# Kernel tuning notes

Measured on AMD Instinct MI355X. Metric: run time of the kernel, lower is better.

The kernel has to match this reference:

```python
import jax, jax.numpy as jnp
import numpy as np

WINDOW = 7
TOKEN_SELF_ATTN_VALUE = -5e4  # from lucidrains local-attention
LN_EPS = 1e-5


def _layer_norm(x, g, b):
    mu = jnp.mean(x, axis=-1, keepdims=True)
    var = jnp.mean(jnp.square(x - mu), axis=-1, keepdims=True)
    return (x - mu) * jax.lax.rsqrt(var + LN_EPS) * g + b


def _local_attention(q, k, v, window):
    # q,k,v: (b, n, d); shared_qk=True, causal=True, look_backward=1, look_forward=0
    b, n, d = q.shape
    nw = n // window
    scale = d ** -0.5
    # shared_qk: l2-normalize keys (torch F.normalize eps=1e-12)
    k = k / jnp.maximum(jnp.linalg.norm(k, axis=-1, keepdims=True), 1e-12)
    bq = q.reshape(b, nw, window, d) * scale
    bk = k.reshape(b, nw, window, d)
    bv = v.reshape(b, nw, window, d)
    # look_around: previous window + current window -> (b, nw, 2w, d)
    prev_k = jnp.pad(bk, ((0, 0), (1, 0), (0, 0), (0, 0)))[:, :nw]
    prev_v = jnp.pad(bv, ((0, 0), (1, 0), (0, 0), (0, 0)))[:, :nw]
    bk2 = jnp.concatenate([prev_k, bk], axis=2)
    bv2 = jnp.concatenate([prev_v, bv], axis=2)
    # absolute positions; padded positions marked -1
    t = jnp.arange(n).reshape(nw, window)             # (nw, w)
    prev_t = jnp.pad(t, ((1, 0), (0, 0)), constant_values=-1)[:nw]
    tk = jnp.concatenate([prev_t, t], axis=1)          # (nw, 2w)
    sim = jnp.einsum('bnie,bnje->bnij', bq, bk2)       # (b, nw, w, 2w)
    self_mask = t[:, :, None] == tk[:, None, :]
    sim = jnp.where(self_mask, TOKEN_SELF_ATTN_VALUE, sim)
    invalid = (t[:, :, None] < tk[:, None, :]) | (tk[:, None, :] == -1)
    sim = jnp.where(invalid, -jnp.finfo(sim.dtype).max, sim)
    attn = jax.nn.softmax(sim, axis=-1)
    out = jnp.einsum('bnij,bnjd->bnid', attn, bv2)
    return out.reshape(b, n, d)


def setup_inputs() -> dict:
    key = jax.random.key(0)
    ks = jax.random.split(key, 10)
    B, H, W, C = 8, 112, 112, 256
    s = 1.0 / np.sqrt(C)
    return {
        'x': jax.random.normal(ks[0], (B, H, W, C), dtype=jnp.float32),
        'ln_g': jnp.ones((C,), jnp.float32),
        'ln_b': jnp.zeros((C,), jnp.float32),
        'wq_w': jax.random.uniform(ks[1], (C, C), jnp.float32, -s, s),
        'wq_b': jax.random.uniform(ks[2], (C,), jnp.float32, -s, s),
        'wk_w': jax.random.uniform(ks[3], (C, C), jnp.float32, -s, s),
        'wk_b': jax.random.uniform(ks[4], (C,), jnp.float32, -s, s),
        'wv_w': jax.random.uniform(ks[5], (C, C), jnp.float32, -s, s),
        'wv_b': jax.random.uniform(ks[6], (C,), jnp.float32, -s, s),
        'mlp_w': jax.random.uniform(ks[7], (C, C), jnp.float32, -s, s),
        'mlp_b': jax.random.uniform(ks[8], (C,), jnp.float32, -s, s),
    }


def reference(x, ln_g, ln_b, wq_w, wq_b, wk_w, wk_b, wv_w, wv_b, mlp_w, mlp_b):
    B, H, W, C = x.shape
    shift = WINDOW // 2  # int(7/2) = 3
    xs = jnp.roll(x, (shift, shift), axis=(1, 2))
    xs = _layer_norm(xs, ln_g, ln_b)
    flat = xs.reshape(B, H * W, C)
    q = flat @ wq_w.T + wq_b
    k = flat @ wk_w.T + wk_b
    v = flat @ wv_w.T + wv_b
    attn_out = _local_attention(q, k, v, WINDOW).reshape(B, H, W, C)
    x_unshifted = jnp.roll(attn_out, (-shift, -shift), axis=(1, 2))
    residual = x_unshifted + x
    xn = _layer_norm(residual, ln_g, ln_b)  # same LN params (module reused)
    flat2 = xn.reshape(B, H * W, C)
    mlp = jax.nn.gelu(flat2 @ mlp_w.T + mlp_b, approximate=False).reshape(B, H, W, C)
    return mlp + residual
```

## Files before the change

kernel.cpp:

```cpp
#include <hip/hip_runtime.h>

#define NTOK 100352
#define NPB  12544
#define CH   256

typedef unsigned short u16;
typedef float f32x4 __attribute__((ext_vector_type(4)));
typedef short bfrag __attribute__((ext_vector_type(8)));

static __device__ __forceinline__ u16 f2bf(float f) {
    union { float f; unsigned u; } v; v.f = f;
    unsigned r = v.u + 0x7FFFu + ((v.u >> 16) & 1u);
    return (u16)(r >> 16);
}
static __device__ __forceinline__ float bf2f(u16 h) {
    union { unsigned u; float f; } v; v.u = ((unsigned)h) << 16;
    return v.f;
}
static __device__ __forceinline__ unsigned pk2(float a, float b) {
    return (unsigned)f2bf(a) | ((unsigned)f2bf(b) << 16);
}
static __device__ __forceinline__ void gl16(const u16* g, u16* l) {
    __builtin_amdgcn_global_load_lds(
        (const __attribute__((address_space(1))) void*)g,
        (__attribute__((address_space(3))) void*)l, 16, 0, 0);
}
static __device__ __forceinline__ float gelu_fast(float v) {
    float z = v * 0.70710678118654752f;
    float a = fabsf(z);
    float t = 1.0f / fmaf(0.3275911f, a, 1.0f);
    float p = t * fmaf(t, fmaf(t, fmaf(t, fmaf(t, 1.061405429f, -1.453152027f),
                                        1.421413741f), -0.284496736f), 0.254829592f);
    float e = __expf(-a * a);
    float erfa = fmaf(-p, e, 1.0f);
    float erfz = (z < 0.f) ? -erfa : erfa;
    return 0.5f * v * (1.0f + erfz);
}

__global__ __launch_bounds__(256)
void swa_prep(const float* __restrict__ wq, const float* __restrict__ wk,
              const float* __restrict__ wv, const float* __restrict__ wm,
              u16* __restrict__ wcat, u16* __restrict__ wmb)
{
    int i0 = blockIdx.x * 256 + threadIdx.x;
    int stride = gridDim.x * 256;
    for (int i = i0; i < 768 * 256; i += stride) {
        int r = i >> 8, c = i & 255;
        float v;
        if (r < 256)      v = wq[r * 256 + c] * 0.0625f;
        else if (r < 512) v = wk[(r - 256) * 256 + c];
        else              v = wv[(r - 512) * 256 + c];
        wcat[i] = f2bf(v);
    }
    for (int i = i0; i < 256 * 256; i += stride) wmb[i] = f2bf(wm[i]);
}

__global__ __launch_bounds__(256)
void swa_ln(const float* __restrict__ x,
            const float* __restrict__ ln_g, const float* __restrict__ ln_b,
            u16* __restrict__ xn)
{
    const int lane = threadIdx.x & 63;
    const int wid  = threadIdx.x >> 6;
    f32x4 lg = *reinterpret_cast<const f32x4*>(ln_g + lane * 4);
    f32x4 lb = *reinterpret_cast<const f32x4*>(ln_b + lane * 4);

    const int wtok0 = (blockIdx.x * 4 + wid) * 16;
    for (int i = 0; i < 16; ++i) {
        int tok = wtok0 + i;
        int b_  = tok / NPB;
        int rem = tok - b_ * NPB;
        int h = rem / 112, w = rem - h * 112;
        int h0 = h - 3 + ((h < 3) ? 112 : 0);
        int w0 = w - 3 + ((w < 3) ? 112 : 0);
        f32x4 v = *reinterpret_cast<const f32x4*>(x + (size_t)(b_ * NPB + h0 * 112 + w0) * CH + lane * 4);
        float s  = v[0] + v[1] + v[2] + v[3];
        float sq = v[0]*v[0] + v[1]*v[1] + v[2]*v[2] + v[3]*v[3];
        #pragma unroll
        for (int m = 1; m < 64; m <<= 1) { s += __shfl_xor(s, m); sq += __shfl_xor(sq, m); }
        float mu  = s * (1.0f / 256.0f);
        float var = sq * (1.0f / 256.0f) - mu * mu;
        float inv = 1.0f / sqrtf(var + 1e-5f);
        uint2 p;
        p.x = pk2((v[0] - mu) * inv * lg[0] + lb[0], (v[1] - mu) * inv * lg[1] + lb[1]);
        p.y = pk2((v[2] - mu) * inv * lg[2] + lb[2], (v[3] - mu) * inv * lg[3] + lb[3]);
        *reinterpret_cast<uint2*>(xn + (size_t)tok * CH + lane * 4) = p;
    }
}

__global__ __launch_bounds__(512)
void swa_kv(const u16* __restrict__ xn, const u16* __restrict__ wcat,
            const float* __restrict__ bk, const float* __restrict__ bv,
            u16* __restrict__ kbuf, u16* __restrict__ vbuf)
{
    __shared__ u16 wt[128 * 256];

    const int tid  = threadIdx.x;
    const int lane = tid & 63;
    const int wid  = tid >> 6;
    const int r16  = lane & 15, g4 = lane >> 4;
    const int swz   = (blockIdx.x & 7) * 196 + (blockIdx.x >> 3);
    const int type  = swz / 392;
    const int strip = swz % 392;
    const int sec   = 1 + (type >> 1);
    const int half  = type & 1;
    const int tok0w = strip * 256 + wid * 32;
    const int wrow0 = sec * 256 + half * 128;

    #pragma unroll
    for (int rr2 = 0; rr2 < 8; ++rr2) {
        int o   = (tid + rr2 * 512) * 16;
        int row = o >> 9;
        int cp  = (o >> 4) & 31;
        int c   = (cp & 24) | ((cp & 7) ^ (row & 7));
        gl16(wcat + (size_t)(wrow0 + row) * CH + c * 8, wt + o / 2);
    }

    bfrag bx[2][8];
    #pragma unroll
    for (int fj = 0; fj < 2; ++fj) {
        const u16* xp = xn + (size_t)(tok0w + fj * 16 + r16) * CH + g4 * 8;
        #pragma unroll
        for (int kb = 0; kb < 8; ++kb)
            bx[fj][kb] = *reinterpret_cast<const bfrag*>(xp + kb * 32);
    }

    u16*         outp = (sec == 1) ? kbuf : vbuf;
    const float* bsp  = (sec == 1) ? bk : bv;

    __syncthreads();

    #pragma unroll
    for (int p = 0; p < 4; ++p) {
        f32x4 acc[2][2];
        #pragma unroll
        for (int ct = 0; ct < 2; ++ct) { acc[ct][0] = (f32x4)0.f; acc[ct][1] = (f32x4)0.f; }
        #pragma unroll
        for (int kk = 0; kk < 8; ++kk) {
            bfrag af[2];
            #pragma unroll
            for (int ct = 0; ct < 2; ++ct) {
                int row = p * 32 + ct * 16 + r16;
                int cc  = kk * 4 + g4;
                int cp  = (cc & 24) | ((cc & 7) ^ (row & 7));
                af[ct]  = *reinterpret_cast<const bfrag*>((const char*)wt + row * 512 + cp * 16);
            }
            #pragma unroll
            for (int ct = 0; ct < 2; ++ct) {
                acc[ct][0] = __builtin_amdgcn_mfma_f32_16x16x32_bf16(af[ct], bx[0][kk], acc[ct][0], 0, 0, 0);
                acc[ct][1] = __builtin_amdgcn_mfma_f32_16x16x32_bf16(af[ct], bx[1][kk], acc[ct][1], 0, 0, 0);
            }
        }
        #pragma unroll
        for (int ct = 0; ct < 2; ++ct) {
            int ch = half * 128 + p * 32 + ct * 16 + g4 * 4;
            f32x4 bb = *reinterpret_cast<const f32x4*>(bsp + ch);
            #pragma unroll
            for (int fj = 0; fj < 2; ++fj) {
                int tok = tok0w + fj * 16 + r16;
                uint2 pkk;
                pkk.x = pk2(acc[ct][fj][0] + bb[0], acc[ct][fj][1] + bb[1]);
                pkk.y = pk2(acc[ct][fj][2] + bb[2], acc[ct][fj][3] + bb[3]);
                *reinterpret_cast<uint2*>(outp + (size_t)tok * CH + ch) = pkk;
            }
        }
    }
}

__global__ __launch_bounds__(512)
void swa_q(u16* xnq, const u16* __restrict__ wcat, const float* __restrict__ bq)
{
    __shared__ u16 wt[256 * 256];

    const int tid  = threadIdx.x;
    const int lane = tid & 63;
    const int wid  = tid >> 6;
    const int r16  = lane & 15, g4 = lane >> 4;
    const int strip = (blockIdx.x & 7) * 49 + (blockIdx.x >> 3);
    const int tok0w = strip * 256 + wid * 32;

    #pragma unroll
    for (int rr2 = 0; rr2 < 16; ++rr2) {
        int o   = (tid + rr2 * 512) * 16;
        int row = o >> 9;
        int cp  = (o >> 4) & 31;
        int c   = (cp & 24) | ((cp & 7) ^ (row & 7));
        gl16(wcat + (size_t)row * CH + c * 8, wt + o / 2);
    }

    bfrag bx[2][8];
    #pragma unroll
    for (int fj = 0; fj < 2; ++fj) {
        const u16* xp = xnq + (size_t)(tok0w + fj * 16 + r16) * CH + g4 * 8;
        #pragma unroll
        for (int kb = 0; kb < 8; ++kb)
            bx[fj][kb] = *reinterpret_cast<const bfrag*>(xp + kb * 32);
    }

    __syncthreads();

    #pragma unroll
    for (int p = 0; p < 8; ++p) {
        f32x4 acc[2][2];
        #pragma unroll
        for (int ct = 0; ct < 2; ++ct) { acc[ct][0] = (f32x4)0.f; acc[ct][1] = (f32x4)0.f; }
        #pragma unroll
        for (int kk = 0; kk < 8; ++kk) {
            bfrag af[2];
            #pragma unroll
            for (int ct = 0; ct < 2; ++ct) {
                int row = p * 32 + ct * 16 + r16;
                int cc  = kk * 4 + g4;
                int cp  = (cc & 24) | ((cc & 7) ^ (row & 7));
                af[ct]  = *reinterpret_cast<const bfrag*>((const char*)wt + row * 512 + cp * 16);
            }
            #pragma unroll
            for (int ct = 0; ct < 2; ++ct) {
                acc[ct][0] = __builtin_amdgcn_mfma_f32_16x16x32_bf16(af[ct], bx[0][kk], acc[ct][0], 0, 0, 0);
                acc[ct][1] = __builtin_amdgcn_mfma_f32_16x16x32_bf16(af[ct], bx[1][kk], acc[ct][1], 0, 0, 0);
            }
        }
        #pragma unroll
        for (int ct = 0; ct < 2; ++ct) {
            int ch = p * 32 + ct * 16 + g4 * 4;
            f32x4 bb = *reinterpret_cast<const f32x4*>(bq + ch);
            #pragma unroll
            for (int fj = 0; fj < 2; ++fj) {
                int tok = tok0w + fj * 16 + r16;
                uint2 pkk;
                pkk.x = pk2(acc[ct][fj][0] + bb[0] * 0.0625f, acc[ct][fj][1] + bb[1] * 0.0625f);
                pkk.y = pk2(acc[ct][fj][2] + bb[2] * 0.0625f, acc[ct][fj][3] + bb[3] * 0.0625f);
                *reinterpret_cast<uint2*>(xnq + (size_t)tok * CH + ch) = pkk;
            }
        }
    }
}

__global__ __launch_bounds__(256)
void swa_attn(const u16* qbuf, const u16* kbuf, const u16* vbuf, u16* obuf)
{
    __shared__ float plds[4][16][17];
    const int tid  = threadIdx.x;
    const int lane = tid & 63;
    const int wid  = tid >> 6;
    const int win  = blockIdx.x * 4 + wid;
    const int iw   = win % 1792;
    const int base = win * 7;
    const int r16  = lane & 15;
    const int g4   = lane >> 4;

    int qrow = base + r16; if (qrow > NTOK - 1) qrow = NTOK - 1;
    int krow = base - 7 + r16; if (krow < 0) krow = 0;
    const u16* qp = qbuf + (size_t)qrow * CH + g4 * 8;
    const u16* kp = kbuf + (size_t)krow * CH + g4 * 8;

    bfrag kf[8];
    #pragma unroll
    for (int kk = 0; kk < 8; ++kk) kf[kk] = *reinterpret_cast<const bfrag*>(kp + kk * 32);
    float sq = 0.f;
    #pragma unroll
    for (int kk = 0; kk < 8; ++kk)
        #pragma unroll
        for (int e = 0; e < 8; ++e) { float kv = bf2f((u16)kf[kk][e]); sq += kv * kv; }
    sq += __shfl_xor(sq, 16); sq += __shfl_xor(sq, 32);
    float invk = 1.0f / fmaxf(sqrtf(sq), 1e-12f);

    f32x4 s4 = {0.f, 0.f, 0.f, 0.f};
    #pragma unroll
    for (int kk = 0; kk < 8; ++kk) {
        bfrag a = *reinterpret_cast<const bfrag*>(qp + kk * 32);
        s4 = __builtin_amdgcn_mfma_f32_16x16x32_bf16(a, kf[kk], s4, 0, 0, 0);
    }

    const int  j     = r16;
    const bool first = (iw == 0);
    #pragma unroll
    for (int rr = 0; rr < 4; ++rr) {
        int i = g4 * 4 + rr;
        float s = s4[rr] * invk;
        if (j == i + 7) s = -5.0e4f;
        if (j > i + 7 || j >= 14 || (first && j < 7)) s = -3.0e38f;
        s4[rr] = s;
    }
    f32x4 mx = s4;
    #pragma unroll
    for (int off = 8; off; off >>= 1) {
        #pragma unroll
        for (int rr = 0; rr < 4; ++rr) mx[rr] = fmaxf(mx[rr], __shfl_xor(mx[rr], off));
    }
    f32x4 p;
    #pragma unroll
    for (int rr = 0; rr < 4; ++rr) p[rr] = __expf(s4[rr] - mx[rr]);
    f32x4 sm = p;
    #pragma unroll
    for (int off = 8; off; off >>= 1) {
        #pragma unroll
        for (int rr = 0; rr < 4; ++rr) sm[rr] += __shfl_xor(sm[rr], off);
    }
    #pragma unroll
    for (int rr = 0; rr < 4; ++rr) plds[wid][g4 * 4 + rr][j] = p[rr] / sm[rr];
    __syncthreads();

    f32x4 zero4 = {0.f, 0.f, 0.f, 0.f};
    f32x4 oa[7];
    #pragma unroll
    for (int i = 0; i < 7; ++i) oa[i] = zero4;
    for (int jj = 0; jj < 14; ++jj) {
        int vrow = base - 7 + jj;
        if (vrow < 0) vrow = 0;
        ushort4 vr = *reinterpret_cast<const ushort4*>(vbuf + (size_t)vrow * CH + lane * 4);
        f32x4 vvv; vvv[0] = bf2f(vr.x); vvv[1] = bf2f(vr.y); vvv[2] = bf2f(vr.z); vvv[3] = bf2f(vr.w);
        #pragma unroll
        for (int i = 0; i < 7; ++i) {
            float pp = plds[wid][i][jj];
            oa[i][0] += pp * vvv[0]; oa[i][1] += pp * vvv[1];
            oa[i][2] += pp * vvv[2]; oa[i][3] += pp * vvv[3];
        }
    }
    #pragma unroll
    for (int i = 0; i < 7; ++i) {
        ushort4 o; o.x = f2bf(oa[i][0]); o.y = f2bf(oa[i][1]); o.z = f2bf(oa[i][2]); o.w = f2bf(oa[i][3]);
        *reinterpret_cast<ushort4*>(obuf + (size_t)(base + i) * CH + lane * 4) = o;
    }
}

__global__ __launch_bounds__(256)
void swa_mlp6(const float* __restrict__ x, const u16* __restrict__ abuf,
              const float* __restrict__ ln_g, const float* __restrict__ ln_b,
              const u16* __restrict__ wmb, const float* __restrict__ mbias,
              float* __restrict__ out)
{
    __shared__ u16 xs[32 * 264];
    __shared__ u16 rsdl[32 * 264];
    __shared__ float bias[256];
    const int tid  = threadIdx.x;
    const int lane = tid & 63;
    const int wid  = tid >> 6;
    const int tok0 = blockIdx.x * 32;
    const int r16  = lane & 15;
    const int g4   = lane >> 4;

    bias[tid] = mbias[tid];

    {
        const int r   = tid >> 3;
        const int sub = tid & 7;
        int tok = tok0 + r;
        int b_  = tok / NPB, rem = tok - b_ * NPB;
        int h = rem / 112, w = rem - h * 112;
        int hs = h + 3;  if (hs >= 112) hs -= 112;
        int ws_ = w + 3; if (ws_ >= 112) ws_ -= 112;
        const float* xrow = x + (size_t)tok * CH;
        const u16*   arow = abuf + (size_t)(b_ * NPB + hs * 112 + ws_) * CH;

        f32x4 rv[8];
        float s = 0.f, sq = 0.f;
        #pragma unroll
        for (int j = 0; j < 8; ++j) {
            int cf = sub + 8 * j;
            f32x4   xv = *reinterpret_cast<const f32x4*>(xrow + cf * 4);
            ushort4 av = *reinterpret_cast<const ushort4*>(arow + cf * 4);
            rv[j][0] = xv[0] + bf2f(av.x); rv[j][1] = xv[1] + bf2f(av.y);
            rv[j][2] = xv[2] + bf2f(av.z); rv[j][3] = xv[3] + bf2f(av.w);
            s  += rv[j][0] + rv[j][1] + rv[j][2] + rv[j][3];
            sq += rv[j][0]*rv[j][0] + rv[j][1]*rv[j][1] + rv[j][2]*rv[j][2] + rv[j][3]*rv[j][3];
        }
        s += __shfl_xor(s, 1); sq += __shfl_xor(sq, 1);
        s += __shfl_xor(s, 2); sq += __shfl_xor(sq, 2);
        s += __shfl_xor(s, 4); sq += __shfl_xor(sq, 4);
        float mu  = s * (1.0f / 256.0f);
        float var = sq * (1.0f / 256.0f) - mu * mu;
        float inv = 1.0f / sqrtf(var + 1e-5f);

        char* xb = (char*)xs;
        char* rb = (char*)rsdl;
        #pragma unroll
        for (int j = 0; j < 8; ++j) {
            int cf = sub + 8 * j;
            f32x4 g = *reinterpret_cast<const f32x4*>(ln_g + cf * 4);
            f32x4 b = *reinterpret_cast<const f32x4*>(ln_b + cf * 4);
            uint2 px, pr;
            px.x = pk2((rv[j][0]-mu)*inv*g[0]+b[0], (rv[j][1]-mu)*inv*g[1]+b[1]);
            px.y = pk2((rv[j][2]-mu)*inv*g[2]+b[2], (rv[j][3]-mu)*inv*g[3]+b[3]);
            pr.x = pk2(rv[j][0], rv[j][1]);
            pr.y = pk2(rv[j][2], rv[j][3]);
            *reinterpret_cast<uint2*>(xb + r * 528 + cf * 8) = px;
            *reinterpret_cast<uint2*>(rb + r * 528 + cf * 8) = pr;
        }
    }
    __syncthreads();

    f32x4 acc[4][2];
    #pragma unroll
    for (int i = 0; i < 4; ++i) { acc[i][0] = (f32x4)0.f; acc[i][1] = (f32x4)0.f; }

    #pragma unroll
    for (int kk = 0; kk < 8; ++kk) {
        bfrag b0 = *reinterpret_cast<const bfrag*>((const char*)xs + r16 * 528 + kk * 64 + g4 * 16);
        bfrag b1 = *reinterpret_cast<const bfrag*>((const char*)xs + (16 + r16) * 528 + kk * 64 + g4 * 16);
        #pragma unroll
        for (int ct = 0; ct < 4; ++ct) {
            bfrag wf = *reinterpret_cast<const bfrag*>(wmb + (size_t)(wid * 64 + ct * 16 + r16) * CH + kk * 32 + g4 * 8);
            acc[ct][0] = __builtin_amdgcn_mfma_f32_16x16x32_bf16(wf, b0, acc[ct][0], 0, 0, 0);
            acc[ct][1] = __builtin_amdgcn_mfma_f32_16x16x32_bf16(wf, b1, acc[ct][1], 0, 0, 0);
        }
    }

    #pragma unroll
    for (int ct = 0; ct < 4; ++ct) {
        int ch = wid * 64 + ct * 16 + g4 * 4;
        f32x4 bb = *reinterpret_cast<const f32x4*>(&bias[ch]);
        #pragma unroll
        for (int rt = 0; rt < 2; ++rt) {
            int tokL = rt * 16 + r16;
            ushort4 rbv = *reinterpret_cast<const ushort4*>((const char*)rsdl + tokL * 528 + ch * 2);
            f32x4 vv;
            vv[0] = gelu_fast(acc[ct][rt][0] + bb[0]) + bf2f(rbv.x);
            vv[1] = gelu_fast(acc[ct][rt][1] + bb[1]) + bf2f(rbv.y);
            vv[2] = gelu_fast(acc[ct][rt][2] + bb[2]) + bf2f(rbv.z);
            vv[3] = gelu_fast(acc[ct][rt][3] + bb[3]) + bf2f(rbv.w);
            *reinterpret_cast<f32x4*>(out + (size_t)(tok0 + tokL) * CH + ch) = vv;
        }
    }
}

extern "C" void kernel_launch(void* const* d_in, const int* in_sizes, int n_in,
                              void* d_out, int out_size, void* d_ws, size_t ws_size,
                              hipStream_t stream)
{
    const float* x     = (const float*)d_in[0];
    const float* ln_g  = (const float*)d_in[1];
    const float* ln_b  = (const float*)d_in[2];
    const float* wq_w  = (const float*)d_in[3];
    const float* wq_b  = (const float*)d_in[4];
    const float* wk_w  = (const float*)d_in[5];
    const float* wk_b  = (const float*)d_in[6];
    const float* wv_w  = (const float*)d_in[7];
    const float* wv_b  = (const float*)d_in[8];
    const float* mlp_w = (const float*)d_in[9];
    const float* mlp_b = (const float*)d_in[10];

    char* ws = (char*)d_ws;
    u16* wcat = (u16*)ws;
    u16* wmb  = (u16*)(ws + 393216);
    u16* xnq  = (u16*)(ws + 524288);
    u16* kbuf = (u16*)d_out;
    u16* vbuf = (u16*)d_out + (size_t)NTOK * CH;

    swa_prep <<<256,  256, 0, stream>>>(wq_w, wk_w, wv_w, mlp_w, wcat, wmb);
    swa_ln   <<<1568, 256, 0, stream>>>(x, ln_g, ln_b, xnq);
    swa_kv   <<<1568, 512, 0, stream>>>(xnq, wcat, wk_b, wv_b, kbuf, vbuf);
    swa_q    <<<392,  512, 0, stream>>>(xnq, wcat, wq_b);
    swa_attn <<<3584, 256, 0, stream>>>(xnq, kbuf, vbuf, xnq);
    swa_mlp6 <<<3136, 256, 0, stream>>>(x, xnq, ln_g, ln_b, wmb, mlp_b, (float*)d_out);
}
```

Before: 264.9 us.

## Enlarge MLP tile to 64 tokens with 8 waves and swizzle block order

```diff
diff --git a/kernel.cpp b/kernel.cpp
--- a/kernel.cpp
+++ b/kernel.cpp
@@ -324,23 +324,24 @@
     }
 }
 
-__global__ __launch_bounds__(256)
-void swa_mlp6(const float* __restrict__ x, const u16* __restrict__ abuf,
+__global__ __launch_bounds__(512)
+void swa_mlp8(const float* __restrict__ x, const u16* __restrict__ abuf,
               const float* __restrict__ ln_g, const float* __restrict__ ln_b,
               const u16* __restrict__ wmb, const float* __restrict__ mbias,
               float* __restrict__ out)
 {
-    __shared__ u16 xs[32 * 264];
-    __shared__ u16 rsdl[32 * 264];
+    __shared__ u16 xs[64 * 264];
+    __shared__ u16 rsdl[64 * 264];
     __shared__ float bias[256];
     const int tid  = threadIdx.x;
     const int lane = tid & 63;
     const int wid  = tid >> 6;
-    const int tok0 = blockIdx.x * 32;
     const int r16  = lane & 15;
     const int g4   = lane >> 4;
-
-    bias[tid] = mbias[tid];
+    const int swz  = (blockIdx.x & 7) * 196 + (blockIdx.x >> 3);
+    const int tok0 = swz * 64;
+
+    if (tid < 256) bias[tid] = mbias[tid];
 
     {
         const int r   = tid >> 3;
@@ -390,35 +391,40 @@
     }
     __syncthreads();
 
-    f32x4 acc[4][2];
-    #pragma unroll
-    for (int i = 0; i < 4; ++i) { acc[i][0] = (f32x4)0.f; acc[i][1] = (f32x4)0.f; }
+    f32x4 acc[2][4];
+    #pragma unroll
+    for (int ct = 0; ct < 2; ++ct)
+        #pragma unroll
+        for (int fj = 0; fj < 4; ++fj) acc[ct][fj] = (f32x4)0.f;
 
     #pragma unroll
     for (int kk = 0; kk < 8; ++kk) {
-        bfrag b0 = *reinterpret_cast<const bfrag*>((const char*)xs + r16 * 528 + kk * 64 + g4 * 16);
-        bfrag b1 = *reinterpret_cast<const bfrag*>((const char*)xs + (16 + r16) * 528 + kk * 64 + g4 * 16);
-        #pragma unroll
-        for (int ct = 0; ct < 4; ++ct) {
-            bfrag wf = *reinterpret_cast<const bfrag*>(wmb + (size_t)(wid * 64 + ct * 16 + r16) * CH + kk * 32 + g4 * 8);
-            acc[ct][0] = __builtin_amdgcn_mfma_f32_16x16x32_bf16(wf, b0, acc[ct][0], 0, 0, 0);
-            acc[ct][1] = __builtin_amdgcn_mfma_f32_16x16x32_bf16(wf, b1, acc[ct][1], 0, 0, 0);
-        }
-    }
-
-    #pragma unroll
-    for (int ct = 0; ct < 4; ++ct) {
-        int ch = wid * 64 + ct * 16 + g4 * 4;
+        bfrag bfj[4];
+        #pragma unroll
+        for (int fj = 0; fj < 4; ++fj)
+            bfj[fj] = *reinterpret_cast<const bfrag*>((const char*)xs + (fj * 16 + r16) * 528 + kk * 64 + g4 * 16);
+        #pragma unroll
+        for (int ct = 0; ct < 2; ++ct) {
+            bfrag wf = *reinterpret_cast<const bfrag*>(wmb + (size_t)(wid * 32 + ct * 16 + r16) * CH + kk * 32 + g4 * 8);
+            #pragma unroll
+            for (int fj = 0; fj < 4; ++fj)
+                acc[ct][fj] = __builtin_amdgcn_mfma_f32_16x16x32_bf16(wf, bfj[fj], acc[ct][fj], 0, 0, 0);
+        }
+    }
+
+    #pragma unroll
+    for (int ct = 0; ct < 2; ++ct) {
+        int ch = wid * 32 + ct * 16 + g4 * 4;
         f32x4 bb = *reinterpret_cast<const f32x4*>(&bias[ch]);
         #pragma unroll
-        for (int rt = 0; rt < 2; ++rt) {
-            int tokL = rt * 16 + r16;
+        for (int fj = 0; fj < 4; ++fj) {
+            int tokL = fj * 16 + r16;
             ushort4 rbv = *reinterpret_cast<const ushort4*>((const char*)rsdl + tokL * 528 + ch * 2);
             f32x4 vv;
-            vv[0] = gelu_fast(acc[ct][rt][0] + bb[0]) + bf2f(rbv.x);
-            vv[1] = gelu_fast(acc[ct][rt][1] + bb[1]) + bf2f(rbv.y);
-            vv[2] = gelu_fast(acc[ct][rt][2] + bb[2]) + bf2f(rbv.z);
-            vv[3] = gelu_fast(acc[ct][rt][3] + bb[3]) + bf2f(rbv.w);
+            vv[0] = gelu_fast(acc[ct][fj][0] + bb[0]) + bf2f(rbv.x);
+            vv[1] = gelu_fast(acc[ct][fj][1] + bb[1]) + bf2f(rbv.y);
+            vv[2] = gelu_fast(acc[ct][fj][2] + bb[2]) + bf2f(rbv.z);
+            vv[3] = gelu_fast(acc[ct][fj][3] + bb[3]) + bf2f(rbv.w);
             *reinterpret_cast<f32x4*>(out + (size_t)(tok0 + tokL) * CH + ch) = vv;
         }
     }
@@ -452,5 +458,5 @@
     swa_kv   <<<1568, 512, 0, stream>>>(xnq, wcat, wk_b, wv_b, kbuf, vbuf);
     swa_q    <<<392,  512, 0, stream>>>(xnq, wcat, wq_b);
     swa_attn <<<3584, 256, 0, stream>>>(xnq, kbuf, vbuf, xnq);
-    swa_mlp6 <<<3136, 256, 0, stream>>>(x, xnq, ln_g, ln_b, wmb, mlp_b, (float*)d_out);
-}
+    swa_mlp8 <<<1568, 512, 0, stream>>>(x, xnq, ln_g, ln_b, wmb, mlp_b, (float*)d_out);
+}
```

After: 249.6 us. -5.8%, faster.
